# Kernel optimization log

Measured on AMD Instinct MI355X. Metric: run time of the kernel, lower is better.

## Reference

```python
import jax, jax.numpy as jnp
import numpy as np

SPARSITY = 0.1  # fraction of entries kept (set to 1)


def _subnet(scores, k):
    # Mirrors GetSubnet.forward: full sort of flattened |scores|, zero the
    # lowest j = int((1-k)*n) ranks, set the rest to 1 (ties broken by sort order).
    flat = scores.ravel()
    n = flat.size
    j = int((1.0 - k) * n)  # static python int
    order = jnp.argsort(flat)  # ascending
    out = jnp.zeros((n,), dtype=scores.dtype).at[order[j:]].set(1)
    return out.reshape(scores.shape)


def setup_inputs() -> dict:
    key = jax.random.key(0)
    kA, kB = jax.random.split(key)
    # kaiming_uniform_(a=sqrt(5)) => U(-bound, bound), bound = sqrt(6/((1+5)*fan_in)) = 1/sqrt(fan_in)
    A_shape = (1024, 16384)
    B_shape = (16384, 1024)
    bA = 1.0 / np.sqrt(A_shape[1])
    bB = 1.0 / np.sqrt(B_shape[1])
    lora_A_mask = jax.random.uniform(kA, A_shape, jnp.float32, -bA, bA)
    lora_B_mask = jax.random.uniform(kB, B_shape, jnp.float32, -bB, bB)
    return {"lora_A_mask": lora_A_mask, "lora_B_mask": lora_B_mask}


def reference(lora_A_mask, lora_B_mask):
    mask_A = _subnet(jnp.abs(lora_A_mask), SPARSITY)
    mask_B = _subnet(jnp.abs(lora_B_mask), SPARSITY)
    return (mask_A, mask_B)
```

## Files before the change

kernel.cpp:

```cpp
#include <hip/hip_runtime.h>
#include <stdint.h>

#define OFF_SH     0u
#define OFF_H1     16384u
#define OFF_H2     18432u
#define OFF_H3     20480u
#define OFF_G      21504u
#define OFF_CNT    21505u
#define OFF_PREFIX 21506u
#define OFF_RANK   21507u
#define OFF_T      21508u
#define OFF_C      21509u
#define OFF_TCNT   21510u
#define OFF_BCNT   21512u
#define OFF_TBUF   22024u
#define TCAP       8192u
#define MAT_WORDS  (22024u + 2u * TCAP)
#define INIT_WORDS 22024u
#define NB         512
#define SEGCAP     16384u

__global__ void init_k(uint32_t* __restrict__ ws) {
  uint32_t i = blockIdx.x * blockDim.x + threadIdx.x;
  if (i < INIT_WORDS) { ws[i] = 0u; ws[MAT_WORDS + i] = 0u; }
}

__global__ void sample_k(const float* __restrict__ A, const float* __restrict__ B,
                         uint32_t* __restrict__ ws, int nvec) {
  const int m = blockIdx.y;
  const float4* __restrict__ src = (const float4*)(m == 0 ? A : B);
  uint32_t* W = ws + (size_t)m * MAT_WORDS;
  __shared__ uint32_t sh[16384];
  for (int i = threadIdx.x; i < 16384; i += blockDim.x) sh[i] = 0u;
  __syncthreads();
  const int w = threadIdx.x >> 6, lane = threadIdx.x & 63;
  const int cstride = nvec / 256;
  for (int it = 0; it < 4; it++) {
    int chunk = blockIdx.x * 16 + it * 4 + w;
    int fi = chunk * cstride + lane;
    if (fi < nvec) {
      float4 f = src[fi];
      const float v[4] = {f.x, f.y, f.z, f.w};
#pragma unroll
      for (int c = 0; c < 4; c++) {
        uint32_t u = __float_as_uint(v[c]) & 0x7fffffffu;
        atomicAdd(&sh[u >> 17], 1u);
      }
    }
  }
  __syncthreads();
  for (int b = threadIdx.x; b < 16384; b += blockDim.x)
    if (sh[b]) atomicAdd(&W[OFF_SH + b], sh[b]);
}

__global__ void scanG_k(uint32_t* __restrict__ ws, uint32_t need) {
  const int m = blockIdx.x;
  uint32_t* W = ws + (size_t)m * MAT_WORDS;
  __shared__ uint32_t ps[256];
  __shared__ int sbest;
  const int t = threadIdx.x;
  if (t == 0) sbest = -1;
  uint32_t sum = 0u;
  for (int k = 0; k < 64; k++) sum += W[OFF_SH + t * 64 + k];
  ps[t] = sum;
  __syncthreads();
  for (int off = 1; off < 256; off <<= 1) {
    uint32_t v = (t >= off) ? ps[t - off] : 0u;
    __syncthreads();
    ps[t] += v;
    __syncthreads();
  }
  uint32_t total = ps[255];
  uint32_t cum = ps[t] - sum;
  int best = -1;
  for (int k = 0; k < 64; k++) {
    int b = t * 64 + k;
    if (total - cum >= need) best = b;
    cum += W[OFF_SH + b];
  }
  if (best >= 0) atomicMax(&sbest, best);
  __syncthreads();
  if (t == 0) W[OFF_G] = (sbest >= 0) ? ((uint32_t)sbest << 17) : 0u;
}

__global__ void compact_k(const float* __restrict__ A, const float* __restrict__ B,
                          uint32_t* __restrict__ ws, uint32_t* __restrict__ outbuf,
                          int nvec) {
  const int m = blockIdx.y;
  const float4* __restrict__ src = (const float4*)(m == 0 ? A : B);
  uint32_t* W = ws + (size_t)m * MAT_WORDS;
  uint2* __restrict__ seg = (uint2*)(outbuf + (size_t)m * 16777216u) + (size_t)blockIdx.x * SEGCAP;
  __shared__ uint32_t segn;
  if (threadIdx.x == 0) segn = 0u;
  const uint32_t G = W[OFF_G];
  __syncthreads();
  int idx0 = blockIdx.x * blockDim.x + threadIdx.x;
  int stride = gridDim.x * blockDim.x;
  for (int i = idx0; i < nvec; i += stride) {
    float4 f = src[i];
    const float v[4] = {f.x, f.y, f.z, f.w};
    uint32_t cu[4], ci[4], tc = 0u;
#pragma unroll
    for (int c = 0; c < 4; c++) {
      uint32_t u = __float_as_uint(v[c]) & 0x7fffffffu;
      if (u >= G) { cu[tc] = u; ci[tc] = (uint32_t)i * 4u + (uint32_t)c; tc++; }
    }
    if (tc) {
      uint32_t s = atomicAdd(&segn, tc);
      for (uint32_t k = 0; k < tc; k++)
        if (s + k < SEGCAP) seg[s + k] = make_uint2(ci[k], cu[k]);
    }
  }
  __syncthreads();
  if (threadIdx.x == 0) {
    uint32_t c = segn; if (c > SEGCAP) c = SEGCAP;
    W[OFF_BCNT + blockIdx.x] = c;
    atomicAdd(&W[OFF_CNT], c);
  }
}

__global__ void hist1b_k(uint32_t* __restrict__ ws, const uint32_t* __restrict__ outbuf) {
  const int m = blockIdx.y;
  uint32_t* W = ws + (size_t)m * MAT_WORDS;
  const uint2* __restrict__ seg = (const uint2*)(outbuf + (size_t)m * 16777216u) + (size_t)blockIdx.x * SEGCAP;
  __shared__ uint32_t h[2048 * 4];
  for (int i = threadIdx.x; i < 2048 * 4; i += blockDim.x) h[i] = 0u;
  uint32_t n = W[OFF_BCNT + blockIdx.x];
  __syncthreads();
  const uint32_t sub = threadIdx.x & 3u;
  for (uint32_t e = threadIdx.x; e < n; e += blockDim.x) {
    uint2 v = seg[e];
    atomicAdd(&h[(v.y >> 21) * 4u + sub], 1u);
  }
  __syncthreads();
  for (int b = threadIdx.x; b < 2048; b += blockDim.x) {
    uint32_t s = h[b * 4] + h[b * 4 + 1] + h[b * 4 + 2] + h[b * 4 + 3];
    if (s) atomicAdd(&W[OFF_H1 + b], s);
  }
}

__global__ void scan1_k(uint32_t* __restrict__ ws, uint32_t keep) {
  const int m = blockIdx.x;
  uint32_t* W = ws + (size_t)m * MAT_WORDS;
  __shared__ uint32_t h[2048];
  __shared__ uint32_t ps[256];
  const int t = threadIdx.x;
  uint32_t cnt = W[OFF_CNT];
  uint32_t r = cnt - keep;
  uint32_t s = 0u;
  for (int k = 0; k < 8; k++) {
    int b = t * 8 + k;
    uint32_t v = W[OFF_H1 + b];
    h[b] = v; s += v;
  }
  ps[t] = s;
  __syncthreads();
  for (int off = 1; off < 256; off <<= 1) {
    uint32_t v = (t >= off) ? ps[t - off] : 0u;
    __syncthreads();
    ps[t] += v;
    __syncthreads();
  }
  uint32_t base = (t == 0) ? 0u : ps[t - 1];
  for (int k = 0; k < 8; k++) {
    int b = t * 8 + k;
    uint32_t c = h[b];
    if (r >= base && r < base + c) {
      W[OFF_PREFIX] = (uint32_t)b << 21;
      W[OFF_RANK]   = r - base;
    }
    base += c;
  }
}

__global__ void hist2b_k(uint32_t* __restrict__ ws, const uint32_t* __restrict__ outbuf) {
  const int m = blockIdx.y;
  uint32_t* W = ws + (size_t)m * MAT_WORDS;
  const uint2* __restrict__ seg = (const uint2*)(outbuf + (size_t)m * 16777216u) + (size_t)blockIdx.x * SEGCAP;
  __shared__ uint32_t h[2048 * 4];
  for (int i = threadIdx.x; i < 2048 * 4; i += blockDim.x) h[i] = 0u;
  uint32_t n = W[OFF_BCNT + blockIdx.x];
  uint32_t p21 = W[OFF_PREFIX] >> 21;
  __syncthreads();
  const uint32_t sub = threadIdx.x & 3u;
  for (uint32_t e = threadIdx.x; e < n; e += blockDim.x) {
    uint2 v = seg[e];
    if ((v.y >> 21) == p21) atomicAdd(&h[((v.y >> 10) & 2047u) * 4u + sub], 1u);
  }
  __syncthreads();
  for (int b = threadIdx.x; b < 2048; b += blockDim.x) {
    uint32_t s = h[b * 4] + h[b * 4 + 1] + h[b * 4 + 2] + h[b * 4 + 3];
    if (s) atomicAdd(&W[OFF_H2 + b], s);
  }
}

__global__ void scan2_k(uint32_t* __restrict__ ws) {
  const int m = blockIdx.x;
  uint32_t* W = ws + (size_t)m * MAT_WORDS;
  __shared__ uint32_t h[2048];
  __shared__ uint32_t ps[256];
  const int t = threadIdx.x;
  uint32_t r = W[OFF_RANK];
  uint32_t prefix = W[OFF_PREFIX];
  uint32_t s = 0u;
  for (int k = 0; k < 8; k++) {
    int b = t * 8 + k;
    uint32_t v = W[OFF_H2 + b];
    h[b] = v; s += v;
  }
  ps[t] = s;
  __syncthreads();
  for (int off = 1; off < 256; off <<= 1) {
    uint32_t v = (t >= off) ? ps[t - off] : 0u;
    __syncthreads();
    ps[t] += v;
    __syncthreads();
  }
  uint32_t base = (t == 0) ? 0u : ps[t - 1];
  for (int k = 0; k < 8; k++) {
    int b = t * 8 + k;
    uint32_t c = h[b];
    if (r >= base && r < base + c) {
      W[OFF_PREFIX] = prefix | ((uint32_t)b << 10);
      W[OFF_RANK]   = r - base;
    }
    base += c;
  }
}

__global__ void pass3b_k(uint32_t* __restrict__ ws, const uint32_t* __restrict__ outbuf) {
  const int m = blockIdx.y;
  uint32_t* W = ws + (size_t)m * MAT_WORDS;
  const uint2* __restrict__ seg = (const uint2*)(outbuf + (size_t)m * 16777216u) + (size_t)blockIdx.x * SEGCAP;
  __shared__ uint32_t h[1024];
  for (int i = threadIdx.x; i < 1024; i += blockDim.x) h[i] = 0u;
  uint32_t n = W[OFF_BCNT + blockIdx.x];
  uint32_t p10 = W[OFF_PREFIX] >> 10;
  __syncthreads();
  for (uint32_t e = threadIdx.x; e < n; e += blockDim.x) {
    uint2 v = seg[e];
    if ((v.y >> 10) == p10) {
      atomicAdd(&h[v.y & 1023u], 1u);
      uint32_t slot = atomicAdd(&W[OFF_TCNT], 1u);
      if (slot < TCAP) { W[OFF_TBUF + 2u * slot] = v.x; W[OFF_TBUF + 2u * slot + 1u] = v.y; }
    }
  }
  __syncthreads();
  for (int b = threadIdx.x; b < 1024; b += blockDim.x)
    if (h[b]) atomicAdd(&W[OFF_H3 + b], h[b]);
}

__global__ void scan3tie_k(uint32_t* __restrict__ ws) {
  const int m = blockIdx.x;
  uint32_t* W = ws + (size_t)m * MAT_WORDS;
  __shared__ uint32_t h[1024];
  __shared__ uint32_t ps[256];
  __shared__ uint32_t sT, sTarget;
  __shared__ uint32_t tie_idx[1024];
  __shared__ uint32_t tie_n;
  const int t = threadIdx.x;
  uint32_t r = W[OFF_RANK];
  uint32_t prefix = W[OFF_PREFIX];
  uint32_t cnt = W[OFF_TCNT]; if (cnt > TCAP) cnt = TCAP;
  if (t == 0) tie_n = 0u;
  uint32_t s = 0u;
  for (int k = 0; k < 4; k++) {
    int b = t * 4 + k;
    uint32_t v = W[OFF_H3 + b];
    h[b] = v; s += v;
  }
  ps[t] = s;
  __syncthreads();
  for (int off = 1; off < 256; off <<= 1) {
    uint32_t v = (t >= off) ? ps[t - off] : 0u;
    __syncthreads();
    ps[t] += v;
    __syncthreads();
  }
  uint32_t base = (t == 0) ? 0u : ps[t - 1];
  for (int k = 0; k < 4; k++) {
    int b = t * 4 + k;
    uint32_t c = h[b];
    if (r >= base && r < base + c) { sT = prefix | (uint32_t)b; sTarget = r - base; }
    base += c;
  }
  __syncthreads();
  const uint32_t T = sT, target = sTarget;
  for (uint32_t c2 = t; c2 < cnt; c2 += 256u) {
    if (W[OFF_TBUF + 2u * c2 + 1u] == T) {
      uint32_t slot = atomicAdd(&tie_n, 1u);
      if (slot < 1024u) tie_idx[slot] = W[OFF_TBUF + 2u * c2];
    }
  }
  __syncthreads();
  uint32_t E2 = tie_n; if (E2 > 1024u) E2 = 1024u;
  for (uint32_t c2 = t; c2 < E2; c2 += 256u) {
    uint32_t xi = tie_idx[c2];
    uint32_t lt = 0u;
    for (uint32_t k2 = 0; k2 < E2; k2++) lt += (tie_idx[k2] < xi) ? 1u : 0u;
    if (lt == target) W[OFF_C] = xi;
  }
  if (t == 0) W[OFF_T] = T;
}

__global__ void mask_k(const float* __restrict__ A, const float* __restrict__ B,
                       float* __restrict__ out, const uint32_t* __restrict__ ws,
                       int nvec, int n) {
  const int m = blockIdx.y;
  const float4* __restrict__ src = (const float4*)(m == 0 ? A : B);
  float4* __restrict__ dst = (float4*)(out + (size_t)m * (size_t)n);
  const uint32_t* W = ws + (size_t)m * MAT_WORDS;
  const uint32_t T = W[OFF_T];
  const uint32_t C = W[OFF_C];
  int idx0 = blockIdx.x * blockDim.x + threadIdx.x;
  int stride = gridDim.x * blockDim.x;
  for (int i = idx0; i < nvec; i += stride) {
    float4 f = src[i];
    const float v[4] = {f.x, f.y, f.z, f.w};
    float r[4];
#pragma unroll
    for (int c = 0; c < 4; c++) {
      uint32_t u = __float_as_uint(v[c]) & 0x7fffffffu;
      uint32_t idx = (uint32_t)i * 4u + (uint32_t)c;
      r[c] = (u > T || (u == T && idx >= C)) ? 1.0f : 0.0f;
    }
    dst[i] = make_float4(r[0], r[1], r[2], r[3]);
  }
}

extern "C" void kernel_launch(void* const* d_in, const int* in_sizes, int n_in,
                              void* d_out, int out_size, void* d_ws, size_t ws_size,
                              hipStream_t stream) {
  const float* A = (const float*)d_in[0];
  const float* B = (const float*)d_in[1];
  float* out = (float*)d_out;
  uint32_t* ws = (uint32_t*)d_ws;
  uint32_t* outbuf = (uint32_t*)d_out;
  const int n = in_sizes[0];
  const int nvec = n / 4;
  const uint32_t j = (uint32_t)((1.0 - 0.1) * (double)n);
  const uint32_t keep = (uint32_t)n - j;
  const uint32_t need = (13u * 65536u) / 100u;

  init_k<<<(INIT_WORDS + 255) / 256, 256, 0, stream>>>(ws);
  sample_k<<<dim3(16, 2), 256, 0, stream>>>(A, B, ws, nvec);
  scanG_k<<<2, 256, 0, stream>>>(ws, need);
  compact_k<<<dim3(NB, 2), 256, 0, stream>>>(A, B, ws, outbuf, nvec);
  hist1b_k<<<dim3(NB, 2), 256, 0, stream>>>(ws, outbuf);
  scan1_k<<<2, 256, 0, stream>>>(ws, keep);
  hist2b_k<<<dim3(NB, 2), 256, 0, stream>>>(ws, outbuf);
  scan2_k<<<2, 256, 0, stream>>>(ws);
  pass3b_k<<<dim3(NB, 2), 256, 0, stream>>>(ws, outbuf);
  scan3tie_k<<<2, 256, 0, stream>>>(ws);
  mask_k<<<dim3(2048, 2), 256, 0, stream>>>(A, B, out, ws, nvec, n);
}
```

Baseline: 378.4 us.

## Fuse scan stages into histogram kernels and build final mask from compacted bitmap

Merges the sample and threshold-scan kernels into one 1024-thread kernel, and folds each per-stage scan into the tail block of its histogram kernel using an atomic completion counter. This removes several small launches. The radix digits are rebalanced to 10/13/8 bits, and the later histogram passes run on fewer blocks that each walk several segments. When the workspace is large enough, the final mask no longer rereads both inputs: a bitmap is scattered from the compacted candidates and then expanded to floats. The exchange is extra grid-wide fence logic, a bitmap index mapping that is tied to specific block and segment geometry, and a fallback path kept for small workspaces.

```diff
diff --git a/kernel.cpp b/kernel.cpp
--- a/kernel.cpp
+++ b/kernel.cpp
@@ -1,42 +1,46 @@
 #include <hip/hip_runtime.h>
 #include <stdint.h>
 
-#define OFF_SH     0u
-#define OFF_H1     16384u
-#define OFF_H2     18432u
-#define OFF_H3     20480u
-#define OFF_G      21504u
-#define OFF_CNT    21505u
-#define OFF_PREFIX 21506u
-#define OFF_RANK   21507u
-#define OFF_T      21508u
-#define OFF_C      21509u
-#define OFF_TCNT   21510u
-#define OFF_BCNT   21512u
-#define OFF_TBUF   22024u
+#define CTRL       27008u
+#define OFF_H1     0u
+#define OFF_H2     1024u
+#define OFF_H3     9216u
+#define OFF_G      9472u
+#define OFF_CNT    9473u
+#define OFF_PREFIX 9474u
+#define OFF_RANK   9475u
+#define OFF_T      9476u
+#define OFF_C      9477u
+#define OFF_TCNT   9478u
+#define OFF_BCNT   9488u
+#define OFF_TBUF   10512u
 #define TCAP       8192u
-#define MAT_WORDS  (22024u + 2u * TCAP)
-#define INIT_WORDS 22024u
-#define NB         512
-#define SEGCAP     16384u
-
-__global__ void init_k(uint32_t* __restrict__ ws) {
-  uint32_t i = blockIdx.x * blockDim.x + threadIdx.x;
-  if (i < INIT_WORDS) { ws[i] = 0u; ws[MAT_WORDS + i] = 0u; }
-}
-
-__global__ void sample_k(const float* __restrict__ A, const float* __restrict__ B,
-                         uint32_t* __restrict__ ws, int nvec) {
-  const int m = blockIdx.y;
+#define T1A        (2u*CTRL + 0u)
+#define T2A        (2u*CTRL + 1u)
+#define T3A        (2u*CTRL + 2u)
+#define BM_OFF     (2u*CTRL + 16u)
+#define NB         1024
+#define SEGCAP     8192u
+#define NB2        128
+
+__global__ __launch_bounds__(1024) void sampleG_k(const float* __restrict__ A,
+                                                  const float* __restrict__ B,
+                                                  uint32_t* __restrict__ ws,
+                                                  int nvec, uint32_t need) {
+  const int m = blockIdx.x;
   const float4* __restrict__ src = (const float4*)(m == 0 ? A : B);
-  uint32_t* W = ws + (size_t)m * MAT_WORDS;
+  uint32_t* W = ws + (size_t)m * CTRL;
   __shared__ uint32_t sh[16384];
-  for (int i = threadIdx.x; i < 16384; i += blockDim.x) sh[i] = 0u;
-  __syncthreads();
-  const int w = threadIdx.x >> 6, lane = threadIdx.x & 63;
+  __shared__ uint32_t ps[1024];
+  __shared__ int sbest;
+  const int t = threadIdx.x;
+  for (int i = t; i < 16384; i += 1024) sh[i] = 0u;
+  if (t == 0) sbest = -1;
+  __syncthreads();
+  const int w = t >> 6, lane = t & 63;
   const int cstride = nvec / 256;
-  for (int it = 0; it < 4; it++) {
-    int chunk = blockIdx.x * 16 + it * 4 + w;
+  for (int it = 0; it < 16; it++) {
+    int chunk = it * 16 + w;
     int fi = chunk * cstride + lane;
     if (fi < nvec) {
       float4 f = src[fi];
@@ -49,47 +53,36 @@
     }
   }
   __syncthreads();
-  for (int b = threadIdx.x; b < 16384; b += blockDim.x)
-    if (sh[b]) atomicAdd(&W[OFF_SH + b], sh[b]);
-}
-
-__global__ void scanG_k(uint32_t* __restrict__ ws, uint32_t need) {
-  const int m = blockIdx.x;
-  uint32_t* W = ws + (size_t)m * MAT_WORDS;
-  __shared__ uint32_t ps[256];
-  __shared__ int sbest;
-  const int t = threadIdx.x;
-  if (t == 0) sbest = -1;
   uint32_t sum = 0u;
-  for (int k = 0; k < 64; k++) sum += W[OFF_SH + t * 64 + k];
+  for (int k = 0; k < 16; k++) sum += sh[t * 16 + k];
   ps[t] = sum;
   __syncthreads();
-  for (int off = 1; off < 256; off <<= 1) {
+  for (int off = 1; off < 1024; off <<= 1) {
     uint32_t v = (t >= off) ? ps[t - off] : 0u;
-    __syncthreads();
-    ps[t] += v;
-    __syncthreads();
-  }
-  uint32_t total = ps[255];
+    __syncthreads(); ps[t] += v; __syncthreads();
+  }
+  uint32_t total = ps[1023];
   uint32_t cum = ps[t] - sum;
   int best = -1;
-  for (int k = 0; k < 64; k++) {
-    int b = t * 64 + k;
+  for (int k = 0; k < 16; k++) {
+    int b = t * 16 + k;
     if (total - cum >= need) best = b;
-    cum += W[OFF_SH + b];
+    cum += sh[b];
   }
   if (best >= 0) atomicMax(&sbest, best);
   __syncthreads();
   if (t == 0) W[OFF_G] = (sbest >= 0) ? ((uint32_t)sbest << 17) : 0u;
 }
 
-__global__ void compact_k(const float* __restrict__ A, const float* __restrict__ B,
-                          uint32_t* __restrict__ ws, uint32_t* __restrict__ outbuf,
-                          int nvec) {
+__global__ __launch_bounds__(256) void compact_k(const float* __restrict__ A,
+                                                 const float* __restrict__ B,
+                                                 uint32_t* __restrict__ ws,
+                                                 uint32_t* __restrict__ outbuf,
+                                                 int nvec, int half_words) {
   const int m = blockIdx.y;
   const float4* __restrict__ src = (const float4*)(m == 0 ? A : B);
-  uint32_t* W = ws + (size_t)m * MAT_WORDS;
-  uint2* __restrict__ seg = (uint2*)(outbuf + (size_t)m * 16777216u) + (size_t)blockIdx.x * SEGCAP;
+  uint32_t* W = ws + (size_t)m * CTRL;
+  uint2* __restrict__ seg = (uint2*)(outbuf + (size_t)m * half_words) + (size_t)blockIdx.x * SEGCAP;
   __shared__ uint32_t segn;
   if (threadIdx.x == 0) segn = 0u;
   const uint32_t G = W[OFF_G];
@@ -119,197 +112,274 @@
   }
 }
 
-__global__ void hist1b_k(uint32_t* __restrict__ ws, const uint32_t* __restrict__ outbuf) {
-  const int m = blockIdx.y;
-  uint32_t* W = ws + (size_t)m * MAT_WORDS;
-  const uint2* __restrict__ seg = (const uint2*)(outbuf + (size_t)m * 16777216u) + (size_t)blockIdx.x * SEGCAP;
-  __shared__ uint32_t h[2048 * 4];
-  for (int i = threadIdx.x; i < 2048 * 4; i += blockDim.x) h[i] = 0u;
-  uint32_t n = W[OFF_BCNT + blockIdx.x];
-  __syncthreads();
-  const uint32_t sub = threadIdx.x & 3u;
-  for (uint32_t e = threadIdx.x; e < n; e += blockDim.x) {
+__global__ __launch_bounds__(256) void hist1b_k(uint32_t* __restrict__ ws,
+                                                const uint32_t* __restrict__ outbuf,
+                                                uint32_t keep, int half_words) {
+  const int m = blockIdx.y;
+  uint32_t* W = ws + (size_t)m * CTRL;
+  const uint2* __restrict__ seg = (const uint2*)(outbuf + (size_t)m * half_words) + (size_t)blockIdx.x * SEGCAP;
+  __shared__ uint32_t h[1024 * 4];
+  __shared__ uint32_t ps[256];
+  __shared__ int is_tail;
+  const int t = threadIdx.x;
+  for (int i = t; i < 1024 * 4; i += 256) h[i] = 0u;
+  uint32_t nseg = W[OFF_BCNT + blockIdx.x];
+  __syncthreads();
+  const uint32_t sub = t & 3u;
+  for (uint32_t e = t; e < nseg; e += 256u) {
     uint2 v = seg[e];
     atomicAdd(&h[(v.y >> 21) * 4u + sub], 1u);
   }
   __syncthreads();
-  for (int b = threadIdx.x; b < 2048; b += blockDim.x) {
+  for (int b = t; b < 1024; b += 256) {
     uint32_t s = h[b * 4] + h[b * 4 + 1] + h[b * 4 + 2] + h[b * 4 + 3];
     if (s) atomicAdd(&W[OFF_H1 + b], s);
   }
-}
-
-__global__ void scan1_k(uint32_t* __restrict__ ws, uint32_t keep) {
-  const int m = blockIdx.x;
-  uint32_t* W = ws + (size_t)m * MAT_WORDS;
-  __shared__ uint32_t h[2048];
+  __threadfence();
+  __syncthreads();
+  if (t == 0) {
+    uint32_t tot = gridDim.x * gridDim.y;
+    is_tail = (__hip_atomic_fetch_add(&ws[T1A], 1u, __ATOMIC_ACQ_REL,
+                                      __HIP_MEMORY_SCOPE_AGENT) == tot - 1u);
+  }
+  __syncthreads();
+  if (!is_tail) return;
+  __threadfence();
+  for (int mm = 0; mm < 2; mm++) {
+    uint32_t* Wm = ws + (size_t)mm * CTRL;
+    uint32_t cnt = __hip_atomic_load(&Wm[OFF_CNT], __ATOMIC_RELAXED, __HIP_MEMORY_SCOPE_AGENT);
+    uint32_t r = cnt - keep;
+    uint32_t s = 0u;
+    for (int k = 0; k < 4; k++) {
+      int b = t * 4 + k;
+      uint32_t v = __hip_atomic_load(&Wm[OFF_H1 + b], __ATOMIC_RELAXED, __HIP_MEMORY_SCOPE_AGENT);
+      h[b] = v; s += v;
+    }
+    ps[t] = s;
+    __syncthreads();
+    for (int off = 1; off < 256; off <<= 1) {
+      uint32_t v = (t >= off) ? ps[t - off] : 0u;
+      __syncthreads(); ps[t] += v; __syncthreads();
+    }
+    uint32_t base = (t == 0) ? 0u : ps[t - 1];
+    for (int k = 0; k < 4; k++) {
+      int b = t * 4 + k;
+      uint32_t c = h[b];
+      if (r >= base && r < base + c) {
+        Wm[OFF_PREFIX] = (uint32_t)b << 21;
+        Wm[OFF_RANK]   = r - base;
+      }
+      base += c;
+    }
+    __syncthreads();
+  }
+}
+
+__global__ __launch_bounds__(256) void hist2b_k(uint32_t* __restrict__ ws,
+                                                const uint32_t* __restrict__ outbuf,
+                                                int half_words) {
+  const int m = blockIdx.y;
+  uint32_t* W = ws + (size_t)m * CTRL;
+  __shared__ uint32_t h[8192];
   __shared__ uint32_t ps[256];
-  const int t = threadIdx.x;
-  uint32_t cnt = W[OFF_CNT];
-  uint32_t r = cnt - keep;
-  uint32_t s = 0u;
-  for (int k = 0; k < 8; k++) {
-    int b = t * 8 + k;
-    uint32_t v = W[OFF_H1 + b];
-    h[b] = v; s += v;
-  }
-  ps[t] = s;
-  __syncthreads();
-  for (int off = 1; off < 256; off <<= 1) {
-    uint32_t v = (t >= off) ? ps[t - off] : 0u;
-    __syncthreads();
-    ps[t] += v;
-    __syncthreads();
-  }
-  uint32_t base = (t == 0) ? 0u : ps[t - 1];
-  for (int k = 0; k < 8; k++) {
-    int b = t * 8 + k;
-    uint32_t c = h[b];
-    if (r >= base && r < base + c) {
-      W[OFF_PREFIX] = (uint32_t)b << 21;
-      W[OFF_RANK]   = r - base;
-    }
-    base += c;
-  }
-}
-
-__global__ void hist2b_k(uint32_t* __restrict__ ws, const uint32_t* __restrict__ outbuf) {
-  const int m = blockIdx.y;
-  uint32_t* W = ws + (size_t)m * MAT_WORDS;
-  const uint2* __restrict__ seg = (const uint2*)(outbuf + (size_t)m * 16777216u) + (size_t)blockIdx.x * SEGCAP;
-  __shared__ uint32_t h[2048 * 4];
-  for (int i = threadIdx.x; i < 2048 * 4; i += blockDim.x) h[i] = 0u;
-  uint32_t n = W[OFF_BCNT + blockIdx.x];
+  __shared__ int is_tail;
+  const int t = threadIdx.x;
+  for (int i = t; i < 8192; i += 256) h[i] = 0u;
   uint32_t p21 = W[OFF_PREFIX] >> 21;
   __syncthreads();
-  const uint32_t sub = threadIdx.x & 3u;
-  for (uint32_t e = threadIdx.x; e < n; e += blockDim.x) {
+  for (int s = 0; s < NB / NB2; s++) {
+    int sb = blockIdx.x * (NB / NB2) + s;
+    const uint2* __restrict__ seg = (const uint2*)(outbuf + (size_t)m * half_words) + (size_t)sb * SEGCAP;
+    uint32_t nseg = W[OFF_BCNT + sb];
+    for (uint32_t e = t; e < nseg; e += 256u) {
+      uint2 v = seg[e];
+      if ((v.y >> 21) == p21) atomicAdd(&h[(v.y >> 8) & 8191u], 1u);
+    }
+  }
+  __syncthreads();
+  for (int b = t; b < 8192; b += 256)
+    if (h[b]) atomicAdd(&W[OFF_H2 + b], h[b]);
+  __threadfence();
+  __syncthreads();
+  if (t == 0) {
+    uint32_t tot = gridDim.x * gridDim.y;
+    is_tail = (__hip_atomic_fetch_add(&ws[T2A], 1u, __ATOMIC_ACQ_REL,
+                                      __HIP_MEMORY_SCOPE_AGENT) == tot - 1u);
+  }
+  __syncthreads();
+  if (!is_tail) return;
+  __threadfence();
+  for (int mm = 0; mm < 2; mm++) {
+    uint32_t* Wm = ws + (size_t)mm * CTRL;
+    uint32_t r = Wm[OFF_RANK];
+    uint32_t prefix = Wm[OFF_PREFIX];
+    uint32_t sum = 0u;
+    for (int k = 0; k < 32; k++) {
+      int b = t * 32 + k;
+      uint32_t v = __hip_atomic_load(&Wm[OFF_H2 + b], __ATOMIC_RELAXED, __HIP_MEMORY_SCOPE_AGENT);
+      h[b] = v; sum += v;
+    }
+    ps[t] = sum;
+    __syncthreads();
+    for (int off = 1; off < 256; off <<= 1) {
+      uint32_t v = (t >= off) ? ps[t - off] : 0u;
+      __syncthreads(); ps[t] += v; __syncthreads();
+    }
+    uint32_t base = (t == 0) ? 0u : ps[t - 1];
+    for (int k = 0; k < 32; k++) {
+      int b = t * 32 + k;
+      uint32_t c = h[b];
+      if (r >= base && r < base + c) {
+        Wm[OFF_PREFIX] = prefix | ((uint32_t)b << 8);
+        Wm[OFF_RANK]   = r - base;
+      }
+      base += c;
+    }
+    __syncthreads();
+  }
+}
+
+__global__ __launch_bounds__(256) void pass3b_k(uint32_t* __restrict__ ws,
+                                                const uint32_t* __restrict__ outbuf,
+                                                int half_words) {
+  const int m = blockIdx.y;
+  uint32_t* W = ws + (size_t)m * CTRL;
+  __shared__ uint32_t h[256];
+  __shared__ uint32_t ps[256];
+  __shared__ int is_tail;
+  __shared__ uint32_t sT, sTarget, tie_n;
+  __shared__ uint32_t tie_idx[1024];
+  const int t = threadIdx.x;
+  h[t] = 0u;
+  uint32_t p8 = W[OFF_PREFIX] >> 8;
+  __syncthreads();
+  for (int s = 0; s < NB / NB2; s++) {
+    int sb = blockIdx.x * (NB / NB2) + s;
+    const uint2* __restrict__ seg = (const uint2*)(outbuf + (size_t)m * half_words) + (size_t)sb * SEGCAP;
+    uint32_t nseg = W[OFF_BCNT + sb];
+    for (uint32_t e = t; e < nseg; e += 256u) {
+      uint2 v = seg[e];
+      if ((v.y >> 8) == p8) {
+        atomicAdd(&h[v.y & 255u], 1u);
+        uint32_t slot = atomicAdd(&W[OFF_TCNT], 1u);
+        if (slot < TCAP) { W[OFF_TBUF + 2u * slot] = v.x; W[OFF_TBUF + 2u * slot + 1u] = v.y; }
+      }
+    }
+  }
+  __syncthreads();
+  if (h[t]) atomicAdd(&W[OFF_H3 + t], h[t]);
+  __threadfence();
+  __syncthreads();
+  if (t == 0) {
+    uint32_t tot = gridDim.x * gridDim.y;
+    is_tail = (__hip_atomic_fetch_add(&ws[T3A], 1u, __ATOMIC_ACQ_REL,
+                                      __HIP_MEMORY_SCOPE_AGENT) == tot - 1u);
+  }
+  __syncthreads();
+  if (!is_tail) return;
+  __threadfence();
+  for (int mm = 0; mm < 2; mm++) {
+    uint32_t* Wm = ws + (size_t)mm * CTRL;
+    uint32_t r = Wm[OFF_RANK];
+    uint32_t prefix = Wm[OFF_PREFIX];
+    if (t == 0) tie_n = 0u;
+    uint32_t c = __hip_atomic_load(&Wm[OFF_H3 + t], __ATOMIC_RELAXED, __HIP_MEMORY_SCOPE_AGENT);
+    h[t] = c;
+    ps[t] = c;
+    __syncthreads();
+    for (int off = 1; off < 256; off <<= 1) {
+      uint32_t v = (t >= off) ? ps[t - off] : 0u;
+      __syncthreads(); ps[t] += v; __syncthreads();
+    }
+    uint32_t base = ps[t] - h[t];
+    if (r >= base && r < base + h[t]) { sT = prefix | (uint32_t)t; sTarget = r - base; }
+    __syncthreads();
+    const uint32_t T = sT, target = sTarget;
+    uint32_t cnt = __hip_atomic_load(&Wm[OFF_TCNT], __ATOMIC_RELAXED, __HIP_MEMORY_SCOPE_AGENT);
+    if (cnt > TCAP) cnt = TCAP;
+    for (uint32_t c2 = t; c2 < cnt; c2 += 256u) {
+      uint32_t uu = __hip_atomic_load(&Wm[OFF_TBUF + 2u * c2 + 1u], __ATOMIC_RELAXED, __HIP_MEMORY_SCOPE_AGENT);
+      if (uu == T) {
+        uint32_t slot = atomicAdd(&tie_n, 1u);
+        if (slot < 1024u)
+          tie_idx[slot] = __hip_atomic_load(&Wm[OFF_TBUF + 2u * c2], __ATOMIC_RELAXED, __HIP_MEMORY_SCOPE_AGENT);
+      }
+    }
+    __syncthreads();
+    uint32_t E2 = tie_n; if (E2 > 1024u) E2 = 1024u;
+    for (uint32_t c2 = t; c2 < E2; c2 += 256u) {
+      uint32_t xi = tie_idx[c2];
+      uint32_t lt = 0u;
+      for (uint32_t k2 = 0; k2 < E2; k2++) lt += (tie_idx[k2] < xi) ? 1u : 0u;
+      if (lt == target) Wm[OFF_C] = xi;
+    }
+    if (t == 0) Wm[OFF_T] = T;
+    __syncthreads();
+  }
+}
+
+__global__ __launch_bounds__(256) void bitmap_k(const uint32_t* __restrict__ ws,
+                                                const uint32_t* __restrict__ outbuf,
+                                                uint32_t* __restrict__ bm_g,
+                                                int half_words, int bmw) {
+  const int m = blockIdx.y;
+  const uint32_t* W = ws + (size_t)m * CTRL;
+  const uint2* __restrict__ seg = (const uint2*)(outbuf + (size_t)m * half_words) + (size_t)blockIdx.x * SEGCAP;
+  uint32_t* __restrict__ gbm = bm_g + (size_t)m * bmw;
+  __shared__ uint32_t bm[512];
+  const int t = threadIdx.x;
+  bm[t] = 0u; bm[t + 256] = 0u;
+  uint32_t nseg = W[OFF_BCNT + blockIdx.x];
+  const uint32_t T = W[OFF_T];
+  const uint32_t C = W[OFF_C];
+  __syncthreads();
+  const uint32_t b = blockIdx.x;
+  for (uint32_t e = t; e < nseg; e += 256u) {
     uint2 v = seg[e];
-    if ((v.y >> 21) == p21) atomicAdd(&h[((v.y >> 10) & 2047u) * 4u + sub], 1u);
-  }
-  __syncthreads();
-  for (int b = threadIdx.x; b < 2048; b += blockDim.x) {
-    uint32_t s = h[b * 4] + h[b * 4 + 1] + h[b * 4 + 2] + h[b * 4 + 3];
-    if (s) atomicAdd(&W[OFF_H2 + b], s);
-  }
-}
-
-__global__ void scan2_k(uint32_t* __restrict__ ws) {
-  const int m = blockIdx.x;
-  uint32_t* W = ws + (size_t)m * MAT_WORDS;
-  __shared__ uint32_t h[2048];
-  __shared__ uint32_t ps[256];
-  const int t = threadIdx.x;
-  uint32_t r = W[OFF_RANK];
-  uint32_t prefix = W[OFF_PREFIX];
-  uint32_t s = 0u;
-  for (int k = 0; k < 8; k++) {
-    int b = t * 8 + k;
-    uint32_t v = W[OFF_H2 + b];
-    h[b] = v; s += v;
-  }
-  ps[t] = s;
-  __syncthreads();
-  for (int off = 1; off < 256; off <<= 1) {
-    uint32_t v = (t >= off) ? ps[t - off] : 0u;
-    __syncthreads();
-    ps[t] += v;
-    __syncthreads();
-  }
-  uint32_t base = (t == 0) ? 0u : ps[t - 1];
-  for (int k = 0; k < 8; k++) {
-    int b = t * 8 + k;
-    uint32_t c = h[b];
-    if (r >= base && r < base + c) {
-      W[OFF_PREFIX] = prefix | ((uint32_t)b << 10);
-      W[OFF_RANK]   = r - base;
-    }
-    base += c;
-  }
-}
-
-__global__ void pass3b_k(uint32_t* __restrict__ ws, const uint32_t* __restrict__ outbuf) {
-  const int m = blockIdx.y;
-  uint32_t* W = ws + (size_t)m * MAT_WORDS;
-  const uint2* __restrict__ seg = (const uint2*)(outbuf + (size_t)m * 16777216u) + (size_t)blockIdx.x * SEGCAP;
-  __shared__ uint32_t h[1024];
-  for (int i = threadIdx.x; i < 1024; i += blockDim.x) h[i] = 0u;
-  uint32_t n = W[OFF_BCNT + blockIdx.x];
-  uint32_t p10 = W[OFF_PREFIX] >> 10;
-  __syncthreads();
-  for (uint32_t e = threadIdx.x; e < n; e += blockDim.x) {
-    uint2 v = seg[e];
-    if ((v.y >> 10) == p10) {
-      atomicAdd(&h[v.y & 1023u], 1u);
-      uint32_t slot = atomicAdd(&W[OFF_TCNT], 1u);
-      if (slot < TCAP) { W[OFF_TBUF + 2u * slot] = v.x; W[OFF_TBUF + 2u * slot + 1u] = v.y; }
-    }
-  }
-  __syncthreads();
-  for (int b = threadIdx.x; b < 1024; b += blockDim.x)
-    if (h[b]) atomicAdd(&W[OFF_H3 + b], h[b]);
-}
-
-__global__ void scan3tie_k(uint32_t* __restrict__ ws) {
-  const int m = blockIdx.x;
-  uint32_t* W = ws + (size_t)m * MAT_WORDS;
-  __shared__ uint32_t h[1024];
-  __shared__ uint32_t ps[256];
-  __shared__ uint32_t sT, sTarget;
-  __shared__ uint32_t tie_idx[1024];
-  __shared__ uint32_t tie_n;
-  const int t = threadIdx.x;
-  uint32_t r = W[OFF_RANK];
-  uint32_t prefix = W[OFF_PREFIX];
-  uint32_t cnt = W[OFF_TCNT]; if (cnt > TCAP) cnt = TCAP;
-  if (t == 0) tie_n = 0u;
-  uint32_t s = 0u;
-  for (int k = 0; k < 4; k++) {
-    int b = t * 4 + k;
-    uint32_t v = W[OFF_H3 + b];
-    h[b] = v; s += v;
-  }
-  ps[t] = s;
-  __syncthreads();
-  for (int off = 1; off < 256; off <<= 1) {
-    uint32_t v = (t >= off) ? ps[t - off] : 0u;
-    __syncthreads();
-    ps[t] += v;
-    __syncthreads();
-  }
-  uint32_t base = (t == 0) ? 0u : ps[t - 1];
-  for (int k = 0; k < 4; k++) {
-    int b = t * 4 + k;
-    uint32_t c = h[b];
-    if (r >= base && r < base + c) { sT = prefix | (uint32_t)b; sTarget = r - base; }
-    base += c;
-  }
-  __syncthreads();
-  const uint32_t T = sT, target = sTarget;
-  for (uint32_t c2 = t; c2 < cnt; c2 += 256u) {
-    if (W[OFF_TBUF + 2u * c2 + 1u] == T) {
-      uint32_t slot = atomicAdd(&tie_n, 1u);
-      if (slot < 1024u) tie_idx[slot] = W[OFF_TBUF + 2u * c2];
-    }
-  }
-  __syncthreads();
-  uint32_t E2 = tie_n; if (E2 > 1024u) E2 = 1024u;
-  for (uint32_t c2 = t; c2 < E2; c2 += 256u) {
-    uint32_t xi = tie_idx[c2];
-    uint32_t lt = 0u;
-    for (uint32_t k2 = 0; k2 < E2; k2++) lt += (tie_idx[k2] < xi) ? 1u : 0u;
-    if (lt == target) W[OFF_C] = xi;
-  }
-  if (t == 0) W[OFF_T] = T;
-}
-
-__global__ void mask_k(const float* __restrict__ A, const float* __restrict__ B,
-                       float* __restrict__ out, const uint32_t* __restrict__ ws,
-                       int nvec, int n) {
+    if (v.y > T || (v.y == T && v.x >= C)) {
+      uint32_t i4 = v.x >> 2;
+      uint32_t k  = i4 >> 18;
+      uint32_t r  = (i4 & 262143u) - b * 256u;
+      uint32_t lp = k * 1024u + r * 4u + (v.x & 3u);
+      atomicOr(&bm[lp >> 5], 1u << (lp & 31u));
+    }
+  }
+  __syncthreads();
+  for (int w = t; w < 512; w += 256) {
+    int kk = w >> 5, ww = w & 31;
+    gbm[b * 32u + ((uint32_t)kk << 15) + (uint32_t)ww] = bm[w];
+  }
+}
+
+__global__ __launch_bounds__(256) void write_k(const uint32_t* __restrict__ bm_g,
+                                               float* __restrict__ out,
+                                               int n, int bmw) {
+  const int m = blockIdx.y;
+  const uint32_t* __restrict__ gbm = bm_g + (size_t)m * bmw;
+  float4* __restrict__ dst = (float4*)(out + (size_t)m * (size_t)n);
+  __shared__ uint32_t wbuf[256];
+  const int t = threadIdx.x;
+  wbuf[t] = gbm[blockIdx.x * 256 + t];
+  __syncthreads();
+  const int f4base = blockIdx.x * 2048;
+#pragma unroll
+  for (int q = 0; q < 8; q++) {
+    int lp4 = q * 256 + t;
+    uint32_t nib = (wbuf[lp4 >> 3] >> ((lp4 & 7) * 4)) & 15u;
+    dst[f4base + lp4] = make_float4((nib & 1u) ? 1.f : 0.f, (nib & 2u) ? 1.f : 0.f,
+                                    (nib & 4u) ? 1.f : 0.f, (nib & 8u) ? 1.f : 0.f);
+  }
+}
+
+__global__ __launch_bounds__(256) void mask_k(const float* __restrict__ A,
+                                              const float* __restrict__ B,
+                                              float* __restrict__ out,
+                                              const uint32_t* __restrict__ ws,
+                                              int nvec, int n) {
   const int m = blockIdx.y;
   const float4* __restrict__ src = (const float4*)(m == 0 ? A : B);
   float4* __restrict__ dst = (float4*)(out + (size_t)m * (size_t)n);
-  const uint32_t* W = ws + (size_t)m * MAT_WORDS;
+  const uint32_t* W = ws + (size_t)m * CTRL;
   const uint32_t T = W[OFF_T];
   const uint32_t C = W[OFF_C];
   int idx0 = blockIdx.x * blockDim.x + threadIdx.x;
@@ -338,19 +408,25 @@
   uint32_t* outbuf = (uint32_t*)d_out;
   const int n = in_sizes[0];
   const int nvec = n / 4;
+  const int half_words = n;
+  const int bmw = n / 32;
   const uint32_t j = (uint32_t)((1.0 - 0.1) * (double)n);
   const uint32_t keep = (uint32_t)n - j;
   const uint32_t need = (13u * 65536u) / 100u;
 
-  init_k<<<(INIT_WORDS + 255) / 256, 256, 0, stream>>>(ws);
-  sample_k<<<dim3(16, 2), 256, 0, stream>>>(A, B, ws, nvec);
-  scanG_k<<<2, 256, 0, stream>>>(ws, need);
-  compact_k<<<dim3(NB, 2), 256, 0, stream>>>(A, B, ws, outbuf, nvec);
-  hist1b_k<<<dim3(NB, 2), 256, 0, stream>>>(ws, outbuf);
-  scan1_k<<<2, 256, 0, stream>>>(ws, keep);
-  hist2b_k<<<dim3(NB, 2), 256, 0, stream>>>(ws, outbuf);
-  scan2_k<<<2, 256, 0, stream>>>(ws);
-  pass3b_k<<<dim3(NB, 2), 256, 0, stream>>>(ws, outbuf);
-  scan3tie_k<<<2, 256, 0, stream>>>(ws);
-  mask_k<<<dim3(2048, 2), 256, 0, stream>>>(A, B, out, ws, nvec, n);
-}
+  const size_t need_ws = ((size_t)BM_OFF + 2u * (size_t)bmw) * 4u;
+  const bool big = ws_size >= need_ws;
+
+  hipMemsetAsync(d_ws, 0, (size_t)BM_OFF * 4u, stream);
+  sampleG_k<<<2, 1024, 0, stream>>>(A, B, ws, nvec, need);
+  compact_k<<<dim3(NB, 2), 256, 0, stream>>>(A, B, ws, outbuf, nvec, half_words);
+  hist1b_k<<<dim3(NB, 2), 256, 0, stream>>>(ws, outbuf, keep, half_words);
+  hist2b_k<<<dim3(NB2, 2), 256, 0, stream>>>(ws, outbuf, half_words);
+  pass3b_k<<<dim3(NB2, 2), 256, 0, stream>>>(ws, outbuf, half_words);
+  if (big) {
+    bitmap_k<<<dim3(NB, 2), 256, 0, stream>>>(ws, outbuf, ws + BM_OFF, half_words, bmw);
+    write_k<<<dim3(n / 8192, 2), 256, 0, stream>>>(ws + BM_OFF, out, n, bmw);
+  } else {
+    mask_k<<<dim3(2048, 2), 256, 0, stream>>>(A, B, out, ws, nvec, n);
+  }
+}
```

New measurement: 562.2 us. 1.49x slower.
